# Kernel tuning notes

Measured on AMD Instinct MI355X. Metric: run time of the kernel, lower is better.

The kernel has to match this reference:

```python
import jax, jax.numpy as jnp
import numpy as np

VOCAB = 32000
DIM = 64


def setup_inputs() -> dict:
    key = jax.random.key(0)
    k1, k2 = jax.random.split(key)
    sequence = jax.random.randint(k1, (16, 2048), 0, VOCAB, dtype=jnp.int64 if jax.config.jax_enable_x64 else jnp.int32)
    weight = jax.random.normal(k2, (VOCAB, DIM), dtype=jnp.float32)
    return {"sequence": sequence, "weight": weight}


def reference(sequence, weight):
    # Embedding gather: [B, S, D]
    embs = weight[sequence]
    # Pairwise synergy bias: [B, S, S], scaled dot product
    bias = jnp.einsum('bsd,btd->bst', embs, embs) / jnp.sqrt(jnp.asarray(DIM, embs.dtype))
    return bias
```

## Files before the change

kernel.cpp:

```cpp
#include <hip/hip_runtime.h>
#include <hip/hip_bf16.h>

#define VOCAB 32000
#define DIM 64
#define NB 16
#define SEQ 2048

typedef __attribute__((ext_vector_type(8))) short bf16x8;
typedef __attribute__((ext_vector_type(4))) float f32x4;

__device__ __forceinline__ unsigned short f2bf(float f) {
    unsigned int u = __builtin_bit_cast(unsigned int, f);
    u = (u + 0x7fffu + ((u >> 16) & 1u)) >> 16;
    return (unsigned short)u;
}

__global__ __launch_bounds__(256) void gather_cvt(
        const int* __restrict__ seq,
        const float* __restrict__ weight,
        unsigned short* __restrict__ embs) {
    int tid = blockIdx.x * 256 + threadIdx.x;
    int token = tid >> 3;
    int c = (tid & 7) * 8;
    int row = seq[token];
    const float* src = weight + (size_t)row * DIM + c;
    unsigned short o[8];
#pragma unroll
    for (int j = 0; j < 8; ++j) o[j] = f2bf(src[j]);
    *reinterpret_cast<bf16x8*>(embs + (size_t)token * DIM + c) =
        *reinterpret_cast<bf16x8*>(o);
}

__global__ __launch_bounds__(256) void synergy_gemm(
        const unsigned short* __restrict__ embs,
        float* __restrict__ out) {
    const int b    = blockIdx.z;
    const int n0   = blockIdx.x * 128;
    const int wave = threadIdx.x >> 6;
    const int lane = threadIdx.x & 63;
    const int m0   = blockIdx.y * 128 + wave * 32;
    const int r    = lane & 15;
    const int q    = lane >> 4;

    const unsigned short* eb = embs + (size_t)b * SEQ * DIM;

    bf16x8 a[2][2], bv[8][2];
#pragma unroll
    for (int mt = 0; mt < 2; ++mt) {
        const unsigned short* p = eb + (size_t)(m0 + mt * 16 + r) * DIM + q * 8;
        a[mt][0] = *reinterpret_cast<const bf16x8*>(p);
        a[mt][1] = *reinterpret_cast<const bf16x8*>(p + 32);
    }
#pragma unroll
    for (int nt = 0; nt < 8; ++nt) {
        const unsigned short* p = eb + (size_t)(n0 + nt * 16 + r) * DIM + q * 8;
        bv[nt][0] = *reinterpret_cast<const bf16x8*>(p);
        bv[nt][1] = *reinterpret_cast<const bf16x8*>(p + 32);
    }

    f32x4 acc[2][8];
#pragma unroll
    for (int mt = 0; mt < 2; ++mt)
#pragma unroll
        for (int nt = 0; nt < 8; ++nt) {
            f32x4 c = {0.f, 0.f, 0.f, 0.f};
            c = __builtin_amdgcn_mfma_f32_16x16x32_bf16(a[mt][0], bv[nt][0], c, 0, 0, 0);
            c = __builtin_amdgcn_mfma_f32_16x16x32_bf16(a[mt][1], bv[nt][1], c, 0, 0, 0);
            acc[mt][nt] = c;
        }

#pragma unroll
    for (int mt = 0; mt < 2; ++mt)
#pragma unroll
        for (int reg = 0; reg < 4; ++reg) {
            int row = m0 + mt * 16 + q * 4 + reg;
            float* orow = out + (size_t)b * SEQ * SEQ + (size_t)row * SEQ + n0;
#pragma unroll
            for (int nt = 0; nt < 8; ++nt)
                orow[nt * 16 + r] = acc[mt][nt][reg] * 0.125f;
        }
}

extern "C" void kernel_launch(void* const* d_in, const int* in_sizes, int n_in,
                              void* d_out, int out_size, void* d_ws, size_t ws_size,
                              hipStream_t stream) {
    const int*   seq    = (const int*)d_in[0];
    const float* weight = (const float*)d_in[1];
    float*       out    = (float*)d_out;
    unsigned short* embs = (unsigned short*)d_ws;

    gather_cvt<<<dim3(262144 / 256), dim3(256), 0, stream>>>(seq, weight, embs);

    synergy_gemm<<<dim3(SEQ / 128, SEQ / 128, NB), dim3(256), 0, stream>>>(embs, out);
}
```

Before: 286.8 us.

## Fuse embedding gather and bf16 conversion into GEMM kernel with nontemporal stores

```diff
diff --git a/kernel.cpp b/kernel.cpp
--- a/kernel.cpp
+++ b/kernel.cpp
@@ -1,7 +1,5 @@
 #include <hip/hip_runtime.h>
-#include <hip/hip_bf16.h>
 
-#define VOCAB 32000
 #define DIM 64
 #define NB 16
 #define SEQ 2048
@@ -15,24 +13,20 @@
     return (unsigned short)u;
 }
 
-__global__ __launch_bounds__(256) void gather_cvt(
+__device__ __forceinline__ bf16x8 load_frag(const float* __restrict__ p) {
+    f32x4 f0 = *reinterpret_cast<const f32x4*>(p);
+    f32x4 f1 = *reinterpret_cast<const f32x4*>(p + 4);
+    bf16x8 o;
+    o[0] = (short)f2bf(f0[0]); o[1] = (short)f2bf(f0[1]);
+    o[2] = (short)f2bf(f0[2]); o[3] = (short)f2bf(f0[3]);
+    o[4] = (short)f2bf(f1[0]); o[5] = (short)f2bf(f1[1]);
+    o[6] = (short)f2bf(f1[2]); o[7] = (short)f2bf(f1[3]);
+    return o;
+}
+
+__global__ __launch_bounds__(256) void synergy_fused(
         const int* __restrict__ seq,
         const float* __restrict__ weight,
-        unsigned short* __restrict__ embs) {
-    int tid = blockIdx.x * 256 + threadIdx.x;
-    int token = tid >> 3;
-    int c = (tid & 7) * 8;
-    int row = seq[token];
-    const float* src = weight + (size_t)row * DIM + c;
-    unsigned short o[8];
-#pragma unroll
-    for (int j = 0; j < 8; ++j) o[j] = f2bf(src[j]);
-    *reinterpret_cast<bf16x8*>(embs + (size_t)token * DIM + c) =
-        *reinterpret_cast<bf16x8*>(o);
-}
-
-__global__ __launch_bounds__(256) void synergy_gemm(
-        const unsigned short* __restrict__ embs,
         float* __restrict__ out) {
     const int b    = blockIdx.z;
     const int n0   = blockIdx.x * 128;
@@ -42,42 +36,53 @@
     const int r    = lane & 15;
     const int q    = lane >> 4;
 
-    const unsigned short* eb = embs + (size_t)b * SEQ * DIM;
+    const int* sb = seq + b * SEQ;
 
-    bf16x8 a[2][2], bv[8][2];
+    int arow[2], brow[8];
+#pragma unroll
+    for (int mt = 0; mt < 2; ++mt) arow[mt] = sb[m0 + mt * 16 + r];
+#pragma unroll
+    for (int nt = 0; nt < 8; ++nt) brow[nt] = sb[n0 + nt * 16 + r];
+
+    bf16x8 a[2][2];
 #pragma unroll
     for (int mt = 0; mt < 2; ++mt) {
-        const unsigned short* p = eb + (size_t)(m0 + mt * 16 + r) * DIM + q * 8;
-        a[mt][0] = *reinterpret_cast<const bf16x8*>(p);
-        a[mt][1] = *reinterpret_cast<const bf16x8*>(p + 32);
-    }
-#pragma unroll
-    for (int nt = 0; nt < 8; ++nt) {
-        const unsigned short* p = eb + (size_t)(n0 + nt * 16 + r) * DIM + q * 8;
-        bv[nt][0] = *reinterpret_cast<const bf16x8*>(p);
-        bv[nt][1] = *reinterpret_cast<const bf16x8*>(p + 32);
+        const float* p = weight + (size_t)arow[mt] * DIM + q * 8;
+        a[mt][0] = load_frag(p);
+        a[mt][1] = load_frag(p + 32);
     }
 
     f32x4 acc[2][8];
 #pragma unroll
-    for (int mt = 0; mt < 2; ++mt)
+    for (int g = 0; g < 2; ++g) {
+        bf16x8 bv[4][2];
 #pragma unroll
-        for (int nt = 0; nt < 8; ++nt) {
-            f32x4 c = {0.f, 0.f, 0.f, 0.f};
-            c = __builtin_amdgcn_mfma_f32_16x16x32_bf16(a[mt][0], bv[nt][0], c, 0, 0, 0);
-            c = __builtin_amdgcn_mfma_f32_16x16x32_bf16(a[mt][1], bv[nt][1], c, 0, 0, 0);
-            acc[mt][nt] = c;
+        for (int t = 0; t < 4; ++t) {
+            const float* p = weight + (size_t)brow[g * 4 + t] * DIM + q * 8;
+            bv[t][0] = load_frag(p);
+            bv[t][1] = load_frag(p + 32);
         }
+#pragma unroll
+        for (int mt = 0; mt < 2; ++mt)
+#pragma unroll
+            for (int t = 0; t < 4; ++t) {
+                f32x4 c = {0.f, 0.f, 0.f, 0.f};
+                c = __builtin_amdgcn_mfma_f32_16x16x32_bf16(a[mt][0], bv[t][0], c, 0, 0, 0);
+                c = __builtin_amdgcn_mfma_f32_16x16x32_bf16(a[mt][1], bv[t][1], c, 0, 0, 0);
+                acc[mt][g * 4 + t] = c;
+            }
+    }
 
 #pragma unroll
     for (int mt = 0; mt < 2; ++mt)
 #pragma unroll
         for (int reg = 0; reg < 4; ++reg) {
             int row = m0 + mt * 16 + q * 4 + reg;
-            float* orow = out + (size_t)b * SEQ * SEQ + (size_t)row * SEQ + n0;
+            float* orow = out + ((size_t)b * SEQ + row) * SEQ + n0;
 #pragma unroll
             for (int nt = 0; nt < 8; ++nt)
-                orow[nt * 16 + r] = acc[mt][nt][reg] * 0.125f;
+                __builtin_nontemporal_store(acc[mt][nt][reg] * 0.125f,
+                                            orow + nt * 16 + r);
         }
 }
 
@@ -87,9 +92,7 @@
     const int*   seq    = (const int*)d_in[0];
     const float* weight = (const float*)d_in[1];
     float*       out    = (float*)d_out;
-    unsigned short* embs = (unsigned short*)d_ws;
+    (void)d_ws; (void)ws_size;
 
-    gather_cvt<<<dim3(262144 / 256), dim3(256), 0, stream>>>(seq, weight, embs);
-
-    synergy_gemm<<<dim3(SEQ / 128, SEQ / 128, NB), dim3(256), 0, stream>>>(embs, out);
+    synergy_fused<<<dim3(SEQ / 128, SEQ / 128, NB), dim3(256), 0, stream>>>(seq, weight, out);
 }
```

Result: slower. 329.2 us (+14.8%).
